# Kernel optimization log

Hardware: AMD Instinct MI355X
Metric: run time of the kernel (lower is better)

The kernel has to match this reference:

```python
import jax, jax.numpy as jnp
import numpy as np

N, E, D = 50000, 600000, 128  # nodes, edges, units (== vert_dim, so no W_adapt)


def glorot(key, shape):
    lim = np.sqrt(6.0 / (shape[0] + shape[1]))
    return jax.random.uniform(key, shape, jnp.float32, -lim, lim)


def setup_inputs() -> dict:
    key = jax.random.key(0)
    ks = jax.random.split(key, 8)
    X = jax.random.normal(ks[0], (N, D), jnp.float32)
    ref_a = jax.random.randint(ks[1], (E,), 0, N, jnp.int32)
    ref_b = jax.random.randint(ks[2], (E,), 0, N, jnp.int32)
    # msg_net: two Dense(D) layers, inner_activation=None (linear)
    W1 = glorot(ks[3], (D, D)); b1 = jnp.zeros((D,), jnp.float32)
    W2 = glorot(ks[4], (D, D)); b2 = jnp.zeros((D,), jnp.float32)
    # keras GRUCell (reset_after=True): kernel [D,3D], recurrent_kernel [D,3D], bias [2,3D]
    gru_kernel = glorot(ks[5], (D, 3 * D))
    gru_rkernel = glorot(ks[6], (D, 3 * D))
    gru_bias = jnp.zeros((2, 3 * D), jnp.float32)
    return {"X": X, "ref_a": ref_a, "ref_b": ref_b,
            "W1": W1, "b1": b1, "W2": W2, "b2": b2,
            "gru_kernel": gru_kernel, "gru_rkernel": gru_rkernel, "gru_bias": gru_bias}


def _ggnn(X, ref_a, ref_b, W1, b1, W2, b2, gru_kernel, gru_rkernel, gru_bias):
    # msg_net (depth=2, linear inner activation)
    X_msg = (X @ W1 + b1) @ W2 + b2                       # [N, D]
    # wl1_convolution, undirected: scatter-add both directions
    agg = jnp.zeros_like(X_msg)
    agg = agg.at[ref_b].add(X_msg[ref_a])                 # a -> b
    agg = agg.at[ref_a].add(X_msg[ref_b])                 # b -> a (directed=False)
    # keras GRUCell update: inputs = agg, state = X  (reset_after=True)
    mx = agg @ gru_kernel + gru_bias[0]                   # [N, 3D]
    mh = X @ gru_rkernel + gru_bias[1]                    # [N, 3D]
    xz, xr, xh = jnp.split(mx, 3, axis=-1)
    rz, rr, rh = jnp.split(mh, 3, axis=-1)
    z = jax.nn.sigmoid(xz + rz)
    r = jax.nn.sigmoid(xr + rr)
    hh = jnp.tanh(xh + r * rh)
    return z * X + (1.0 - z) * hh                         # [N, D]


def reference(X, ref_a, ref_b, W1, b1, W2, b2, gru_kernel, gru_rkernel, gru_bias):
    return _ggnn(X, ref_a, ref_b, W1, b1, W2, b2, gru_kernel, gru_rkernel, gru_bias)
```

## Files before the change

### kernel.cpp

```cpp
#include <hip/hip_runtime.h>
#include <cstdint>
#include <cstddef>

typedef __bf16 bf16x8 __attribute__((ext_vector_type(8)));
typedef float  f32x4  __attribute__((ext_vector_type(4)));
typedef short  s16x8  __attribute__((ext_vector_type(8)));

static __device__ __forceinline__ float bf2f(short s) {
    union { unsigned u; float f; } v;
    v.u = ((unsigned)(unsigned short)s) << 16;
    return v.f;
}
static __device__ __forceinline__ short f2bf(float f) {
    unsigned u = __float_as_uint(f);
    u += 0x7fffu + ((u >> 16) & 1u);
    return (short)(u >> 16);
}
static __device__ __forceinline__ float rcp_(float x) {
    return __builtin_amdgcn_rcpf(x);
}
static __device__ __forceinline__ float sigmoid_(float x) {
    return rcp_(1.0f + __expf(-x));
}
static __device__ __forceinline__ float tanh_(float x) {
    float ax = fabsf(x);
    float e  = __expf(-2.0f * ax);
    float t  = (1.0f - e) * rcp_(1.0f + e);
    return copysignf(t, x);
}

#define MFMA(a, b, c) __builtin_amdgcn_mfma_f32_16x16x32_bf16((a), (b), (c), 0, 0, 0)

static __device__ __forceinline__ int lidx8(int r, int ch) {
    return r * 128 + ((ch ^ (r & 15)) << 3);
}
static __device__ __forceinline__ int lidx(int r, int col) {
    return r * 128 + ((((col >> 3) ^ (r & 15)) << 3) | (col & 7));
}

#define BLOCKS1     256
#define STRIPE_CAP  64
#define BUCKET_REG  (BLOCKS1 * STRIPE_CAP)
#define NODE_CAP    96

static __device__ __forceinline__ s16x8 cvt8(const float* p) {
    f32x4 a0 = *(const f32x4*)(p);
    f32x4 a1 = *(const f32x4*)(p + 4);
    s16x8 v;
    v[0] = f2bf(a0[0]); v[1] = f2bf(a0[1]); v[2] = f2bf(a0[2]); v[3] = f2bf(a0[3]);
    v[4] = f2bf(a1[0]); v[5] = f2bf(a1[1]); v[6] = f2bf(a1[2]); v[7] = f2bf(a1[3]);
    return v;
}

__global__ __launch_bounds__(512) void pass1_msg_kernel(
    const int* __restrict__ ra, const int* __restrict__ rb,
    unsigned* __restrict__ bucketed, int* __restrict__ stripeCnt,
    int E, int CPB, int nbuckets,
    const float* __restrict__ GK, const float* __restrict__ GR,
    short* __restrict__ GKt, short* __restrict__ GRt,
    const float* __restrict__ X,
    const float* __restrict__ W1, const float* __restrict__ b1,
    const float* __restrict__ W2, const float* __restrict__ b2,
    short* __restrict__ msg, int N)
{
    __shared__ short ldsA[64 * 128];
    __shared__ short ldsY[64 * 128];
    __shared__ int cnt[256];
    const int tid = threadIdx.x;

    if ((int)blockIdx.x < BLOCKS1) {
        if (tid < 256) cnt[tid] = 0;

        int i = blockIdx.x * 512 + tid;
        if (i < 49152) {
            int k = i / 384, n = i - k * 384;
            GKt[n * 128 + k] = f2bf(GK[i]);
            GRt[n * 128 + k] = f2bf(GR[i]);
        }
        __syncthreads();

        const int blk = blockIdx.x;
        const int e1 = min(E, (blk + 1) * CPB);
        for (int e = blk * CPB + tid; e < e1; e += 512) {
            int a = ra[e], b = rb[e];
            int ka = a >> 8, kb = b >> 8;
            int r1 = atomicAdd(&cnt[ka], 1);
            if (r1 < STRIPE_CAP)
                bucketed[(size_t)ka * BUCKET_REG + blk * STRIPE_CAP + r1] =
                    ((unsigned)(a & 255) << 16) | (unsigned)b;
            int r2 = atomicAdd(&cnt[kb], 1);
            if (r2 < STRIPE_CAP)
                bucketed[(size_t)kb * BUCKET_REG + blk * STRIPE_CAP + r2] =
                    ((unsigned)(b & 255) << 16) | (unsigned)a;
        }
        __syncthreads();
        if (tid < nbuckets)
            stripeCnt[(size_t)tid * BLOCKS1 + blk] =
                min(cnt[tid], STRIPE_CAP);
        return;
    }

    const int m0   = (blockIdx.x - BLOCKS1) * 64;
    const int lane = tid & 63, wv = tid >> 6;
    const int q = lane >> 4, c = lane & 15;
    const int ncol = wv * 16 + c;

    bf16x8 w1f[4], w2f[4];
#pragma unroll
    for (int ks = 0; ks < 4; ks++) {
        s16x8 v1, v2;
#pragma unroll
        for (int t = 0; t < 8; t++) {
            int k = ks * 32 + q * 8 + t;
            v1[t] = f2bf(W1[(size_t)k * 128 + ncol]);
            v2[t] = f2bf(W2[(size_t)k * 128 + ncol]);
        }
        w1f[ks] = __builtin_bit_cast(bf16x8, v1);
        w2f[ks] = __builtin_bit_cast(bf16x8, v2);
    }

    for (int i = tid; i < 64 * 16; i += 512) {
        int r = i >> 4, ch = i & 15;
        s16x8 v;
        if (m0 + r < N) v = cvt8(X + (size_t)(m0 + r) * 128 + ch * 8);
        else            v = (s16x8)0;
        *(s16x8*)(ldsA + lidx8(r, ch)) = v;
    }
    __syncthreads();

    f32x4 acc[4];
#pragma unroll
    for (int rt = 0; rt < 4; rt++) acc[rt] = (f32x4)0.0f;
#pragma unroll
    for (int ks = 0; ks < 4; ks++) {
        int kc = ks * 4 + q;
#pragma unroll
        for (int rt = 0; rt < 4; rt++) {
            bf16x8 aA = __builtin_bit_cast(bf16x8, *(const s16x8*)(ldsA + lidx8(rt * 16 + c, kc)));
            acc[rt] = MFMA(aA, w1f[ks], acc[rt]);
        }
    }
    float bias1 = b1[ncol];
#pragma unroll
    for (int rt = 0; rt < 4; rt++)
#pragma unroll
        for (int i = 0; i < 4; i++)
            ldsY[lidx(rt * 16 + q * 4 + i, ncol)] = f2bf(acc[rt][i] + bias1);
    __syncthreads();

#pragma unroll
    for (int rt = 0; rt < 4; rt++) acc[rt] = (f32x4)0.0f;
#pragma unroll
    for (int ks = 0; ks < 4; ks++) {
        int kc = ks * 4 + q;
#pragma unroll
        for (int rt = 0; rt < 4; rt++) {
            bf16x8 aY = __builtin_bit_cast(bf16x8, *(const s16x8*)(ldsY + lidx8(rt * 16 + c, kc)));
            acc[rt] = MFMA(aY, w2f[ks], acc[rt]);
        }
    }
    float bias2 = b2[ncol];
#pragma unroll
    for (int rt = 0; rt < 4; rt++)
#pragma unroll
        for (int i = 0; i < 4; i++) {
            int row = m0 + rt * 16 + q * 4 + i;
            if (row < N) msg[(size_t)row * 128 + ncol] = f2bf(acc[rt][i] + bias2);
        }
}

__global__ __launch_bounds__(512) void pass2_kernel(
    const unsigned* __restrict__ bucketed, const int* __restrict__ stripeCnt,
    unsigned short* __restrict__ nbrS, int* __restrict__ counts, int N)
{
    __shared__ int off[256];
    __shared__ int scnt[256];
    const int tid = threadIdx.x;
    const int k = blockIdx.x;
    if (tid < 256) {
        off[tid]  = 0;
        scnt[tid] = stripeCnt[(size_t)k * BLOCKS1 + tid];
    }
    __syncthreads();
    const int lo = k << 8;
    const unsigned* reg = bucketed + (size_t)k * BUCKET_REG;
    for (int i = tid; i < BUCKET_REG; i += 512) {
        int blk = i >> 6, slot = i & (STRIPE_CAP - 1);
        if (slot < scnt[blk]) {
            unsigned e = reg[i];
            int nl = (int)(e >> 16);
            int p  = (int)(e & 0xffffu);
            int r  = atomicAdd(&off[nl], 1);
            if (r < NODE_CAP)
                nbrS[(size_t)(lo + nl) * NODE_CAP + r] = (unsigned short)p;
        }
    }
    __syncthreads();
    int node = lo + tid;
    if (tid < 256 && node < N) counts[node] = min(off[tid], NODE_CAP);
}

__global__ __launch_bounds__(256) void gather_kernel(
    const short* __restrict__ msg, const unsigned short* __restrict__ nbrS,
    const int* __restrict__ counts, short* __restrict__ aggb, int N)
{
    const int lane = threadIdx.x & 63;
    const int node = blockIdx.x * 4 + (threadIdx.x >> 6);
    if (node >= N) return;
    const int g  = lane >> 4;
    const int cl = lane & 15;
    const int s   = node * NODE_CAP;
    const int end = s + counts[node];

    float a[8];
#pragma unroll
    for (int t = 0; t < 8; t++) a[t] = 0.0f;

    int i = s + g;
    for (; i + 12 < end; i += 16) {
        int j0 = (int)nbrS[i];
        int j1 = (int)nbrS[i + 4];
        int j2 = (int)nbrS[i + 8];
        int j3 = (int)nbrS[i + 12];
        s16x8 p0 = *(const s16x8*)(msg + (size_t)j0 * 128 + cl * 8);
        s16x8 p1 = *(const s16x8*)(msg + (size_t)j1 * 128 + cl * 8);
        s16x8 p2 = *(const s16x8*)(msg + (size_t)j2 * 128 + cl * 8);
        s16x8 p3 = *(const s16x8*)(msg + (size_t)j3 * 128 + cl * 8);
#pragma unroll
        for (int t = 0; t < 8; t++) a[t] += bf2f(p0[t]);
#pragma unroll
        for (int t = 0; t < 8; t++) a[t] += bf2f(p1[t]);
#pragma unroll
        for (int t = 0; t < 8; t++) a[t] += bf2f(p2[t]);
#pragma unroll
        for (int t = 0; t < 8; t++) a[t] += bf2f(p3[t]);
    }
    for (; i + 4 < end; i += 8) {
        int j0 = (int)nbrS[i];
        int j1 = (int)nbrS[i + 4];
        s16x8 p0 = *(const s16x8*)(msg + (size_t)j0 * 128 + cl * 8);
        s16x8 p1 = *(const s16x8*)(msg + (size_t)j1 * 128 + cl * 8);
#pragma unroll
        for (int t = 0; t < 8; t++) a[t] += bf2f(p0[t]);
#pragma unroll
        for (int t = 0; t < 8; t++) a[t] += bf2f(p1[t]);
    }
    if (i < end) {
        int j = (int)nbrS[i];
        s16x8 p = *(const s16x8*)(msg + (size_t)j * 128 + cl * 8);
#pragma unroll
        for (int t = 0; t < 8; t++) a[t] += bf2f(p[t]);
    }

#pragma unroll
    for (int t = 0; t < 8; t++) {
        a[t] += __shfl_xor(a[t], 32);
        a[t] += __shfl_xor(a[t], 16);
    }
    if (g == 0) {
        s16x8 o;
#pragma unroll
        for (int t = 0; t < 8; t++) o[t] = f2bf(a[t]);
        *(s16x8*)(aggb + (size_t)node * 128 + cl * 8) = o;
    }
}

__global__ __launch_bounds__(512) void gru_kernel(
    const short* __restrict__ aggb, const float* __restrict__ X,
    const short* __restrict__ GKt, const short* __restrict__ GRt,
    const float* __restrict__ gbias, float* __restrict__ out, int N)
{
    __shared__ short ldsA[64 * 128];
    __shared__ short ldsX[64 * 128];
    const int tid  = threadIdx.x;
    const int m0   = blockIdx.x * 64;
    const int lane = tid & 63, wv = tid >> 6;
    const int q = lane >> 4, c = lane & 15;
    const int ncol = wv * 16 + c;

    bf16x8 bkz[4], bkr[4], bkh[4], brz[4], brr[4], brh[4];
#pragma unroll
    for (int ks = 0; ks < 4; ks++) {
        int ko = ks * 32 + q * 8;
        bkz[ks] = __builtin_bit_cast(bf16x8, *(const s16x8*)(GKt + (size_t)(ncol)       * 128 + ko));
        bkr[ks] = __builtin_bit_cast(bf16x8, *(const s16x8*)(GKt + (size_t)(128 + ncol) * 128 + ko));
        bkh[ks] = __builtin_bit_cast(bf16x8, *(const s16x8*)(GKt + (size_t)(256 + ncol) * 128 + ko));
        brz[ks] = __builtin_bit_cast(bf16x8, *(const s16x8*)(GRt + (size_t)(ncol)       * 128 + ko));
        brr[ks] = __builtin_bit_cast(bf16x8, *(const s16x8*)(GRt + (size_t)(128 + ncol) * 128 + ko));
        brh[ks] = __builtin_bit_cast(bf16x8, *(const s16x8*)(GRt + (size_t)(256 + ncol) * 128 + ko));
    }
    float bz0 = gbias[ncol],       br0 = gbias[128 + ncol],       bh0 = gbias[256 + ncol];
    float bz1 = gbias[384 + ncol], br1 = gbias[384 + 128 + ncol], bh1 = gbias[384 + 256 + ncol];

    for (int i = tid; i < 64 * 16; i += 512) {
        int r = i >> 4, ch = i & 15;
        s16x8 vx, va;
        if (m0 + r < N) {
            vx = cvt8(X + (size_t)(m0 + r) * 128 + ch * 8);
            va = *(const s16x8*)(aggb + (size_t)(m0 + r) * 128 + ch * 8);
        } else { vx = (s16x8)0; va = (s16x8)0; }
        *(s16x8*)(ldsX + lidx8(r, ch)) = vx;
        *(s16x8*)(ldsA + lidx8(r, ch)) = va;
    }
    __syncthreads();

#pragma clang loop unroll(disable)
    for (int rt = 0; rt < 4; rt++) {
        float xv[4];
#pragma unroll
        for (int i = 0; i < 4; i++) {
            int grow = m0 + rt * 16 + q * 4 + i;
            xv[i] = (grow < N) ? X[(size_t)grow * 128 + ncol] : 0.0f;
        }
        f32x4 axz = (f32x4)0.0f, axr = (f32x4)0.0f, axh = (f32x4)0.0f;
        f32x4 arz = (f32x4)0.0f, arr = (f32x4)0.0f, arh = (f32x4)0.0f;
#pragma unroll
        for (int ks = 0; ks < 4; ks++) {
            int kc = ks * 4 + q;
            bf16x8 aA = __builtin_bit_cast(bf16x8, *(const s16x8*)(ldsA + lidx8(rt * 16 + c, kc)));
            bf16x8 aX = __builtin_bit_cast(bf16x8, *(const s16x8*)(ldsX + lidx8(rt * 16 + c, kc)));
            axz = MFMA(aA, bkz[ks], axz);
            axr = MFMA(aA, bkr[ks], axr);
            axh = MFMA(aA, bkh[ks], axh);
            arz = MFMA(aX, brz[ks], arz);
            arr = MFMA(aX, brr[ks], arr);
            arh = MFMA(aX, brh[ks], arh);
        }
#pragma unroll
        for (int i = 0; i < 4; i++) {
            int grow = m0 + rt * 16 + q * 4 + i;
            if (grow < N) {
                float z  = sigmoid_(axz[i] + bz0 + arz[i] + bz1);
                float r  = sigmoid_(axr[i] + br0 + arr[i] + br1);
                float hh = tanh_(axh[i] + bh0 + r * (arh[i] + bh1));
                out[(size_t)grow * 128 + ncol] = z * xv[i] + (1.0f - z) * hh;
            }
        }
    }
}

extern "C" void kernel_launch(void* const* d_in, const int* in_sizes, int n_in,
                              void* d_out, int out_size, void* d_ws, size_t ws_size,
                              hipStream_t stream)
{
    const float* X  = (const float*)d_in[0];
    const int*   ra = (const int*)d_in[1];
    const int*   rb = (const int*)d_in[2];
    const float* W1 = (const float*)d_in[3];
    const float* b1 = (const float*)d_in[4];
    const float* W2 = (const float*)d_in[5];
    const float* b2 = (const float*)d_in[6];
    const float* GK = (const float*)d_in[7];
    const float* GR = (const float*)d_in[8];
    const float* GB = (const float*)d_in[9];
    const int N = in_sizes[0] / 128;
    const int E = in_sizes[1];
    float* out = (float*)d_out;

    const int nbuckets = (N + 255) >> 8;

    char* ws = (char*)d_ws;
    size_t off = 0;
    short* aggb   = (short*)(ws + off);   off += (size_t)N * 128 * 2;
    short* msg    = (short*)(ws + off);   off += (size_t)N * 128 * 2;
    short* GKt    = (short*)(ws + off);   off += 49152u * 2;
    short* GRt    = (short*)(ws + off);   off += 49152u * 2;
    unsigned* bucketed = (unsigned*)(ws + off);
    off += (size_t)nbuckets * BUCKET_REG * 4;
    unsigned short* nbrS = (unsigned short*)(ws + off);
    off += (size_t)nbuckets * 256 * NODE_CAP * 2;
    int* counts    = (int*)(ws + off);    off += (size_t)N * 4;
    int* stripeCnt = (int*)(ws + off);    off += (size_t)nbuckets * BLOCKS1 * 4;

    const int CPB = (E + BLOCKS1 - 1) / BLOCKS1;
    const int nblk64 = (N + 63) / 64;

    pass1_msg_kernel<<<BLOCKS1 + nblk64, 512, 0, stream>>>(
        ra, rb, bucketed, stripeCnt, E, CPB, nbuckets,
        GK, GR, GKt, GRt,
        X, W1, b1, W2, b2, msg, N);

    pass2_kernel<<<nbuckets, 512, 0, stream>>>(bucketed, stripeCnt, nbrS, counts, N);

    gather_kernel<<<(N + 3) / 4, 256, 0, stream>>>(msg, nbrS, counts, aggb, N);

    gru_kernel<<<nblk64, 512, 0, stream>>>(aggb, X, GKt, GRt, GB, out, N);
}
```

Baseline: 203.3 us.

## Build adjacency lists with direct global atomics, dropping the bucketing pass

Replaces the two-stage bucketed adjacency build (LDS-counted stripes followed by a second per-bucket kernel) with a single pass in which each edge atomically claims a slot in the per-node neighbor list via global atomics on a counts array. The counts array is zeroed with a memset, and the gather kernel clamps counts to NODE_CAP. This removes one kernel launch and the intermediate bucketed buffer round-trip. In exchange it issues 1.2M scattered global atomics and random writes, which may contend or cost more than LDS atomics.

```diff
diff --git a/kernel.cpp b/kernel.cpp
--- a/kernel.cpp
+++ b/kernel.cpp
@@ -38,10 +38,8 @@
     return r * 128 + ((((col >> 3) ^ (r & 15)) << 3) | (col & 7));
 }
 
-#define BLOCKS1     256
-#define STRIPE_CAP  64
-#define BUCKET_REG  (BLOCKS1 * STRIPE_CAP)
-#define NODE_CAP    96
+#define NODE_CAP  96
+#define NBUILD    192
 
 static __device__ __forceinline__ s16x8 cvt8(const float* p) {
     f32x4 a0 = *(const f32x4*)(p);
@@ -52,10 +50,9 @@
     return v;
 }
 
-__global__ __launch_bounds__(512) void pass1_msg_kernel(
+__global__ __launch_bounds__(512) void build_msg_kernel(
     const int* __restrict__ ra, const int* __restrict__ rb,
-    unsigned* __restrict__ bucketed, int* __restrict__ stripeCnt,
-    int E, int CPB, int nbuckets,
+    unsigned short* __restrict__ nbrS, int* __restrict__ counts, int E,
     const float* __restrict__ GK, const float* __restrict__ GR,
     short* __restrict__ GKt, short* __restrict__ GRt,
     const float* __restrict__ X,
@@ -65,42 +62,28 @@
 {
     __shared__ short ldsA[64 * 128];
     __shared__ short ldsY[64 * 128];
-    __shared__ int cnt[256];
     const int tid = threadIdx.x;
 
-    if ((int)blockIdx.x < BLOCKS1) {
-        if (tid < 256) cnt[tid] = 0;
-
+    if ((int)blockIdx.x < NBUILD) {
         int i = blockIdx.x * 512 + tid;
         if (i < 49152) {
             int k = i / 384, n = i - k * 384;
             GKt[n * 128 + k] = f2bf(GK[i]);
             GRt[n * 128 + k] = f2bf(GR[i]);
         }
-        __syncthreads();
-
-        const int blk = blockIdx.x;
-        const int e1 = min(E, (blk + 1) * CPB);
-        for (int e = blk * CPB + tid; e < e1; e += 512) {
+        for (int e = blockIdx.x * 512 + tid; e < E; e += NBUILD * 512) {
             int a = ra[e], b = rb[e];
-            int ka = a >> 8, kb = b >> 8;
-            int r1 = atomicAdd(&cnt[ka], 1);
-            if (r1 < STRIPE_CAP)
-                bucketed[(size_t)ka * BUCKET_REG + blk * STRIPE_CAP + r1] =
-                    ((unsigned)(a & 255) << 16) | (unsigned)b;
-            int r2 = atomicAdd(&cnt[kb], 1);
-            if (r2 < STRIPE_CAP)
-                bucketed[(size_t)kb * BUCKET_REG + blk * STRIPE_CAP + r2] =
-                    ((unsigned)(b & 255) << 16) | (unsigned)a;
-        }
-        __syncthreads();
-        if (tid < nbuckets)
-            stripeCnt[(size_t)tid * BLOCKS1 + blk] =
-                min(cnt[tid], STRIPE_CAP);
+            int r1 = atomicAdd(&counts[a], 1);
+            if (r1 < NODE_CAP)
+                nbrS[(size_t)a * NODE_CAP + r1] = (unsigned short)b;
+            int r2 = atomicAdd(&counts[b], 1);
+            if (r2 < NODE_CAP)
+                nbrS[(size_t)b * NODE_CAP + r2] = (unsigned short)a;
+        }
         return;
     }
 
-    const int m0   = (blockIdx.x - BLOCKS1) * 64;
+    const int m0   = (blockIdx.x - NBUILD) * 64;
     const int lane = tid & 63, wv = tid >> 6;
     const int q = lane >> 4, c = lane & 15;
     const int ncol = wv * 16 + c;
@@ -167,37 +150,6 @@
             int row = m0 + rt * 16 + q * 4 + i;
             if (row < N) msg[(size_t)row * 128 + ncol] = f2bf(acc[rt][i] + bias2);
         }
-}
-
-__global__ __launch_bounds__(512) void pass2_kernel(
-    const unsigned* __restrict__ bucketed, const int* __restrict__ stripeCnt,
-    unsigned short* __restrict__ nbrS, int* __restrict__ counts, int N)
-{
-    __shared__ int off[256];
-    __shared__ int scnt[256];
-    const int tid = threadIdx.x;
-    const int k = blockIdx.x;
-    if (tid < 256) {
-        off[tid]  = 0;
-        scnt[tid] = stripeCnt[(size_t)k * BLOCKS1 + tid];
-    }
-    __syncthreads();
-    const int lo = k << 8;
-    const unsigned* reg = bucketed + (size_t)k * BUCKET_REG;
-    for (int i = tid; i < BUCKET_REG; i += 512) {
-        int blk = i >> 6, slot = i & (STRIPE_CAP - 1);
-        if (slot < scnt[blk]) {
-            unsigned e = reg[i];
-            int nl = (int)(e >> 16);
-            int p  = (int)(e & 0xffffu);
-            int r  = atomicAdd(&off[nl], 1);
-            if (r < NODE_CAP)
-                nbrS[(size_t)(lo + nl) * NODE_CAP + r] = (unsigned short)p;
-        }
-    }
-    __syncthreads();
-    int node = lo + tid;
-    if (tid < 256 && node < N) counts[node] = min(off[tid], NODE_CAP);
 }
 
 __global__ __launch_bounds__(256) void gather_kernel(
@@ -210,7 +162,7 @@
     const int g  = lane >> 4;
     const int cl = lane & 15;
     const int s   = node * NODE_CAP;
-    const int end = s + counts[node];
+    const int end = s + min(counts[node], NODE_CAP);
 
     float a[8];
 #pragma unroll
@@ -357,31 +309,25 @@
     const int E = in_sizes[1];
     float* out = (float*)d_out;
 
-    const int nbuckets = (N + 255) >> 8;
-
     char* ws = (char*)d_ws;
     size_t off = 0;
     short* aggb   = (short*)(ws + off);   off += (size_t)N * 128 * 2;
     short* msg    = (short*)(ws + off);   off += (size_t)N * 128 * 2;
     short* GKt    = (short*)(ws + off);   off += 49152u * 2;
     short* GRt    = (short*)(ws + off);   off += 49152u * 2;
-    unsigned* bucketed = (unsigned*)(ws + off);
-    off += (size_t)nbuckets * BUCKET_REG * 4;
     unsigned short* nbrS = (unsigned short*)(ws + off);
-    off += (size_t)nbuckets * 256 * NODE_CAP * 2;
-    int* counts    = (int*)(ws + off);    off += (size_t)N * 4;
-    int* stripeCnt = (int*)(ws + off);    off += (size_t)nbuckets * BLOCKS1 * 4;
-
-    const int CPB = (E + BLOCKS1 - 1) / BLOCKS1;
+    off += (size_t)N * NODE_CAP * 2;
+    int* counts   = (int*)(ws + off);     off += (size_t)N * 4;
+
+    hipMemsetAsync(counts, 0, (size_t)N * 4, stream);
+
     const int nblk64 = (N + 63) / 64;
 
-    pass1_msg_kernel<<<BLOCKS1 + nblk64, 512, 0, stream>>>(
-        ra, rb, bucketed, stripeCnt, E, CPB, nbuckets,
+    build_msg_kernel<<<NBUILD + nblk64, 512, 0, stream>>>(
+        ra, rb, nbrS, counts, E,
         GK, GR, GKt, GRt,
         X, W1, b1, W2, b2, msg, N);
 
-    pass2_kernel<<<nbuckets, 512, 0, stream>>>(bucketed, stripeCnt, nbrS, counts, N);
-
     gather_kernel<<<(N + 3) / 4, 256, 0, stream>>>(msg, nbrS, counts, aggb, N);
 
     gru_kernel<<<nblk64, 512, 0, stream>>>(aggb, X, GKt, GRt, GB, out, N);
```

Result: slower. 234.1 us (+15.2%).

## Fuse CSR build and neighbor gather into one LDS slab kernel with 64-node buckets

Applied to the files above, without the earlier changes.

Buckets shrink from 256 to 64 nodes. The second pass now builds each bucket's neighbor lists in shared memory and gathers messages from them directly, replacing the separate pass2 and gather kernels. This removes the global nbrS/counts round trip and one launch. The trade-off is fewer, heavier gather blocks (~782 blocks of 8 waves, each doing 8 nodes serially), which may cut latency hiding. Stripe capacity is halved to 32 per block per bucket, and cnt grows to 1024 entries.

```diff
diff --git a/kernel.cpp b/kernel.cpp
--- a/kernel.cpp
+++ b/kernel.cpp
@@ -39,7 +39,7 @@
 }
 
 #define BLOCKS1     256
-#define STRIPE_CAP  64
+#define STRIPE_CAP  32
 #define BUCKET_REG  (BLOCKS1 * STRIPE_CAP)
 #define NODE_CAP    96
 
@@ -55,7 +55,7 @@
 __global__ __launch_bounds__(512) void pass1_msg_kernel(
     const int* __restrict__ ra, const int* __restrict__ rb,
     unsigned* __restrict__ bucketed, int* __restrict__ stripeCnt,
-    int E, int CPB, int nbuckets,
+    int E, int CPB, int nbk,
     const float* __restrict__ GK, const float* __restrict__ GR,
     short* __restrict__ GKt, short* __restrict__ GRt,
     const float* __restrict__ X,
@@ -65,11 +65,11 @@
 {
     __shared__ short ldsA[64 * 128];
     __shared__ short ldsY[64 * 128];
-    __shared__ int cnt[256];
+    __shared__ int cnt[1024];
     const int tid = threadIdx.x;
 
     if ((int)blockIdx.x < BLOCKS1) {
-        if (tid < 256) cnt[tid] = 0;
+        for (int b = tid; b < nbk; b += 512) cnt[b] = 0;
 
         int i = blockIdx.x * 512 + tid;
         if (i < 49152) {
@@ -83,20 +83,19 @@
         const int e1 = min(E, (blk + 1) * CPB);
         for (int e = blk * CPB + tid; e < e1; e += 512) {
             int a = ra[e], b = rb[e];
-            int ka = a >> 8, kb = b >> 8;
+            int ka = a >> 6, kb = b >> 6;
             int r1 = atomicAdd(&cnt[ka], 1);
             if (r1 < STRIPE_CAP)
                 bucketed[(size_t)ka * BUCKET_REG + blk * STRIPE_CAP + r1] =
-                    ((unsigned)(a & 255) << 16) | (unsigned)b;
+                    ((unsigned)(a & 63) << 16) | (unsigned)b;
             int r2 = atomicAdd(&cnt[kb], 1);
             if (r2 < STRIPE_CAP)
                 bucketed[(size_t)kb * BUCKET_REG + blk * STRIPE_CAP + r2] =
-                    ((unsigned)(b & 255) << 16) | (unsigned)a;
+                    ((unsigned)(b & 63) << 16) | (unsigned)a;
         }
         __syncthreads();
-        if (tid < nbuckets)
-            stripeCnt[(size_t)tid * BLOCKS1 + blk] =
-                min(cnt[tid], STRIPE_CAP);
+        for (int b = tid; b < nbk; b += 512)
+            stripeCnt[(size_t)b * BLOCKS1 + blk] = min(cnt[b], STRIPE_CAP);
         return;
     }
 
@@ -169,99 +168,93 @@
         }
 }
 
-__global__ __launch_bounds__(512) void pass2_kernel(
+__global__ __launch_bounds__(512) void slab_gather_kernel(
     const unsigned* __restrict__ bucketed, const int* __restrict__ stripeCnt,
-    unsigned short* __restrict__ nbrS, int* __restrict__ counts, int N)
+    const short* __restrict__ msg, short* __restrict__ aggb, int N)
 {
-    __shared__ int off[256];
-    __shared__ int scnt[256];
+    __shared__ unsigned short slab[64 * NODE_CAP];
+    __shared__ int off[64];
+    __shared__ int scnt[BLOCKS1];
     const int tid = threadIdx.x;
-    const int k = blockIdx.x;
-    if (tid < 256) {
-        off[tid]  = 0;
-        scnt[tid] = stripeCnt[(size_t)k * BLOCKS1 + tid];
-    }
-    __syncthreads();
-    const int lo = k << 8;
-    const unsigned* reg = bucketed + (size_t)k * BUCKET_REG;
+    const int b   = blockIdx.x;
+
+    if (tid < 64) off[tid] = 0;
+    if (tid < BLOCKS1) scnt[tid] = stripeCnt[(size_t)b * BLOCKS1 + tid];
+    __syncthreads();
+
+    const unsigned* reg = bucketed + (size_t)b * BUCKET_REG;
     for (int i = tid; i < BUCKET_REG; i += 512) {
-        int blk = i >> 6, slot = i & (STRIPE_CAP - 1);
-        if (slot < scnt[blk]) {
+        if ((i & (STRIPE_CAP - 1)) < scnt[i >> 5]) {
             unsigned e = reg[i];
             int nl = (int)(e >> 16);
             int p  = (int)(e & 0xffffu);
             int r  = atomicAdd(&off[nl], 1);
             if (r < NODE_CAP)
-                nbrS[(size_t)(lo + nl) * NODE_CAP + r] = (unsigned short)p;
-        }
-    }
-    __syncthreads();
-    int node = lo + tid;
-    if (tid < 256 && node < N) counts[node] = min(off[tid], NODE_CAP);
-}
-
-__global__ __launch_bounds__(256) void gather_kernel(
-    const short* __restrict__ msg, const unsigned short* __restrict__ nbrS,
-    const int* __restrict__ counts, short* __restrict__ aggb, int N)
-{
-    const int lane = threadIdx.x & 63;
-    const int node = blockIdx.x * 4 + (threadIdx.x >> 6);
-    if (node >= N) return;
-    const int g  = lane >> 4;
+                slab[nl * NODE_CAP + r] = (unsigned short)p;
+        }
+    }
+    __syncthreads();
+
+    const int lane = tid & 63, wv = tid >> 6;
+    const int q  = lane >> 4;
     const int cl = lane & 15;
-    const int s   = node * NODE_CAP;
-    const int end = s + counts[node];
-
-    float a[8];
-#pragma unroll
-    for (int t = 0; t < 8; t++) a[t] = 0.0f;
-
-    int i = s + g;
-    for (; i + 12 < end; i += 16) {
-        int j0 = (int)nbrS[i];
-        int j1 = (int)nbrS[i + 4];
-        int j2 = (int)nbrS[i + 8];
-        int j3 = (int)nbrS[i + 12];
-        s16x8 p0 = *(const s16x8*)(msg + (size_t)j0 * 128 + cl * 8);
-        s16x8 p1 = *(const s16x8*)(msg + (size_t)j1 * 128 + cl * 8);
-        s16x8 p2 = *(const s16x8*)(msg + (size_t)j2 * 128 + cl * 8);
-        s16x8 p3 = *(const s16x8*)(msg + (size_t)j3 * 128 + cl * 8);
-#pragma unroll
-        for (int t = 0; t < 8; t++) a[t] += bf2f(p0[t]);
-#pragma unroll
-        for (int t = 0; t < 8; t++) a[t] += bf2f(p1[t]);
-#pragma unroll
-        for (int t = 0; t < 8; t++) a[t] += bf2f(p2[t]);
-#pragma unroll
-        for (int t = 0; t < 8; t++) a[t] += bf2f(p3[t]);
-    }
-    for (; i + 4 < end; i += 8) {
-        int j0 = (int)nbrS[i];
-        int j1 = (int)nbrS[i + 4];
-        s16x8 p0 = *(const s16x8*)(msg + (size_t)j0 * 128 + cl * 8);
-        s16x8 p1 = *(const s16x8*)(msg + (size_t)j1 * 128 + cl * 8);
-#pragma unroll
-        for (int t = 0; t < 8; t++) a[t] += bf2f(p0[t]);
-#pragma unroll
-        for (int t = 0; t < 8; t++) a[t] += bf2f(p1[t]);
-    }
-    if (i < end) {
-        int j = (int)nbrS[i];
-        s16x8 p = *(const s16x8*)(msg + (size_t)j * 128 + cl * 8);
-#pragma unroll
-        for (int t = 0; t < 8; t++) a[t] += bf2f(p[t]);
-    }
-
-#pragma unroll
-    for (int t = 0; t < 8; t++) {
-        a[t] += __shfl_xor(a[t], 32);
-        a[t] += __shfl_xor(a[t], 16);
-    }
-    if (g == 0) {
-        s16x8 o;
-#pragma unroll
-        for (int t = 0; t < 8; t++) o[t] = f2bf(a[t]);
-        *(s16x8*)(aggb + (size_t)node * 128 + cl * 8) = o;
+
+    for (int k = 0; k < 8; k++) {
+        const int nl   = wv * 8 + k;
+        const int node = b * 64 + nl;
+        float a[8];
+#pragma unroll
+        for (int t = 0; t < 8; t++) a[t] = 0.0f;
+        if (node < N) {
+            const int deg = min(off[nl], NODE_CAP);
+            const unsigned short* lst = slab + nl * NODE_CAP;
+            int i = q;
+            for (; i + 12 < deg; i += 16) {
+                int j0 = (int)lst[i];
+                int j1 = (int)lst[i + 4];
+                int j2 = (int)lst[i + 8];
+                int j3 = (int)lst[i + 12];
+                s16x8 p0 = *(const s16x8*)(msg + (size_t)j0 * 128 + cl * 8);
+                s16x8 p1 = *(const s16x8*)(msg + (size_t)j1 * 128 + cl * 8);
+                s16x8 p2 = *(const s16x8*)(msg + (size_t)j2 * 128 + cl * 8);
+                s16x8 p3 = *(const s16x8*)(msg + (size_t)j3 * 128 + cl * 8);
+#pragma unroll
+                for (int t = 0; t < 8; t++) a[t] += bf2f(p0[t]);
+#pragma unroll
+                for (int t = 0; t < 8; t++) a[t] += bf2f(p1[t]);
+#pragma unroll
+                for (int t = 0; t < 8; t++) a[t] += bf2f(p2[t]);
+#pragma unroll
+                for (int t = 0; t < 8; t++) a[t] += bf2f(p3[t]);
+            }
+            for (; i + 4 < deg; i += 8) {
+                int j0 = (int)lst[i];
+                int j1 = (int)lst[i + 4];
+                s16x8 p0 = *(const s16x8*)(msg + (size_t)j0 * 128 + cl * 8);
+                s16x8 p1 = *(const s16x8*)(msg + (size_t)j1 * 128 + cl * 8);
+#pragma unroll
+                for (int t = 0; t < 8; t++) a[t] += bf2f(p0[t]);
+#pragma unroll
+                for (int t = 0; t < 8; t++) a[t] += bf2f(p1[t]);
+            }
+            if (i < deg) {
+                int j = (int)lst[i];
+                s16x8 p = *(const s16x8*)(msg + (size_t)j * 128 + cl * 8);
+#pragma unroll
+                for (int t = 0; t < 8; t++) a[t] += bf2f(p[t]);
+            }
+        }
+#pragma unroll
+        for (int t = 0; t < 8; t++) {
+            a[t] += __shfl_xor(a[t], 32);
+            a[t] += __shfl_xor(a[t], 16);
+        }
+        if (q == 0 && b * 64 + nl < N) {
+            s16x8 o;
+#pragma unroll
+            for (int t = 0; t < 8; t++) o[t] = f2bf(a[t]);
+            *(s16x8*)(aggb + (size_t)(b * 64 + nl) * 128 + cl * 8) = o;
+        }
     }
 }
 
@@ -357,7 +350,7 @@
     const int E = in_sizes[1];
     float* out = (float*)d_out;
 
-    const int nbuckets = (N + 255) >> 8;
+    const int nbk = (N + 63) / 64;
 
     char* ws = (char*)d_ws;
     size_t off = 0;
@@ -366,23 +359,17 @@
     short* GKt    = (short*)(ws + off);   off += 49152u * 2;
     short* GRt    = (short*)(ws + off);   off += 49152u * 2;
     unsigned* bucketed = (unsigned*)(ws + off);
-    off += (size_t)nbuckets * BUCKET_REG * 4;
-    unsigned short* nbrS = (unsigned short*)(ws + off);
-    off += (size_t)nbuckets * 256 * NODE_CAP * 2;
-    int* counts    = (int*)(ws + off);    off += (size_t)N * 4;
-    int* stripeCnt = (int*)(ws + off);    off += (size_t)nbuckets * BLOCKS1 * 4;
+    off += (size_t)nbk * BUCKET_REG * 4;
+    int* stripeCnt = (int*)(ws + off);    off += (size_t)nbk * BLOCKS1 * 4;
 
     const int CPB = (E + BLOCKS1 - 1) / BLOCKS1;
-    const int nblk64 = (N + 63) / 64;
-
-    pass1_msg_kernel<<<BLOCKS1 + nblk64, 512, 0, stream>>>(
-        ra, rb, bucketed, stripeCnt, E, CPB, nbuckets,
+
+    pass1_msg_kernel<<<BLOCKS1 + nbk, 512, 0, stream>>>(
+        ra, rb, bucketed, stripeCnt, E, CPB, nbk,
         GK, GR, GKt, GRt,
         X, W1, b1, W2, b2, msg, N);
 
-    pass2_kernel<<<nbuckets, 512, 0, stream>>>(bucketed, stripeCnt, nbrS, counts, N);
-
-    gather_kernel<<<(N + 3) / 4, 256, 0, stream>>>(msg, nbrS, counts, aggb, N);
-
-    gru_kernel<<<nblk64, 512, 0, stream>>>(aggb, X, GKt, GRt, GB, out, N);
-}
+    slab_gather_kernel<<<nbk, 512, 0, stream>>>(bucketed, stripeCnt, msg, aggb, N);
+
+    gru_kernel<<<nbk, 512, 0, stream>>>(aggb, X, GKt, GRt, GB, out, N);
+}
```

New measurement: 200.9 us. No clear change (-1.1%).
